# Optimization experiments

Measured on AMD Instinct MI355X. Metric: run time of the kernel, lower is better.

## Reference

```python
import jax, jax.numpy as jnp
import numpy as np

N = 50000   # nodes
E = 800000  # edges (avg degree 16)
H = 128     # hidden_dim / emb_dim
OUT = 128   # out_dim
NUM_BOND_TYPE = 6
NUM_BOND_DIR = 6


def setup_inputs() -> dict:
    key = jax.random.key(0)
    ks = jax.random.split(key, 12)
    s = 0.05
    return {
        "x": jax.random.normal(ks[0], (N, H), jnp.float32),
        "edge_index": jax.random.randint(ks[1], (2, E), 0, N),
        "edge_attr": jax.random.randint(ks[2], (E, 2), 0, 6),
        "prelu_a": jnp.float32(0.25),  # PReLU single shared slope (torch default)
        "W_enc": jax.random.normal(ks[3], (H, H), jnp.float32) * s,  # enc_to_dec, no bias
        "edge_emb1": jax.random.normal(ks[4], (NUM_BOND_TYPE, H), jnp.float32) * s,
        "edge_emb2": jax.random.normal(ks[5], (NUM_BOND_DIR, H), jnp.float32) * s,
        "W1": jax.random.normal(ks[6], (H, 2 * H), jnp.float32) * s,
        "b1": jnp.zeros((2 * H,), jnp.float32),
        "W2": jax.random.normal(ks[7], (2 * H, OUT), jnp.float32) * s,
        "b2": jnp.zeros((OUT,), jnp.float32),
    }


def reference(x, edge_index, edge_attr, prelu_a, W_enc, edge_emb1, edge_emb2, W1, b1, W2, b2):
    n = x.shape[0]
    # GNNDecoder: PReLU then enc_to_dec linear (no bias)
    x = jnp.where(x > 0, x, prelu_a * x)
    x = x @ W_enc

    # GINConv.forward: add self loops, self-loop edge_attr = [5, 0]
    loop = jnp.arange(n)
    src = jnp.concatenate([edge_index[0], loop])  # [E+N]
    dst = jnp.concatenate([edge_index[1], loop])  # [E+N]
    ea1 = jnp.concatenate([edge_attr[:, 0], jnp.full((n,), 5, edge_attr.dtype)])
    ea2 = jnp.concatenate([edge_attr[:, 1], jnp.zeros((n,), edge_attr.dtype)])

    # edge embedding lookup + gather-add message + scatter-add aggregate
    edge_emb = edge_emb1[ea1] + edge_emb2[ea2]          # [E+N, H]
    msg = x[src] + edge_emb                             # message(x_j, edge_attr)
    agg = jax.ops.segment_sum(msg, dst, num_segments=n)  # aggr='add'

    # update: MLP Linear(H,2H) -> SiLU -> Linear(2H,OUT)
    h = jax.nn.silu(agg @ W1 + b1)
    return h @ W2 + b2
```

## Files before the change

### kernel.cpp

```cpp
#include <hip/hip_runtime.h>

typedef unsigned short u16;
typedef unsigned int   u32;
typedef __attribute__((ext_vector_type(8))) short short8;
typedef __attribute__((ext_vector_type(4))) float f32x4;

#define MAXDEG 64
#define CAP    28
#define EB     4096

__device__ __forceinline__ float bl(u32 u){ union{u32 i; float f;} c; c.i = u << 16; return c.f; }
__device__ __forceinline__ float bh(u32 u){ union{u32 i; float f;} c; c.i = u & 0xffff0000u; return c.f; }
__device__ __forceinline__ u16 f2b(float f){
  union{float f; u32 i;} c; c.f = f;
  return (u16)((c.i + 0x8000u) >> 16);
}
__device__ __forceinline__ u32 pk2(float a, float b){
  union{float f; u32 i;} x, y; x.f = a; y.f = b;
  return ((x.i + 0x8000u) >> 16) | ((y.i + 0x8000u) & 0xffff0000u);
}

__device__ __forceinline__ void tr_tile(
    const float* __restrict__ in, int K, int Nn, u16* __restrict__ out,
    int k0, int n0, int t, u16* __restrict__ sT )
{
  #pragma unroll
  for (int rr = 0; rr < 4; rr++) {
    int row = (t >> 4) + rr * 16;
    int c4  = (t & 15) * 4;
    float4 v = *(const float4*)&in[(size_t)(k0 + row) * Nn + n0 + c4];
    sT[(c4 + 0) * 72 + row] = f2b(v.x);
    sT[(c4 + 1) * 72 + row] = f2b(v.y);
    sT[(c4 + 2) * 72 + row] = f2b(v.z);
    sT[(c4 + 3) * 72 + row] = f2b(v.w);
  }
  __syncthreads();
  #pragma unroll
  for (int ww = 0; ww < 2; ww++) {
    int nn = (t >> 3) + ww * 32;
    int c8 = (t & 7) * 8;
    uint4 val = *(const uint4*)&sT[nn * 72 + c8];
    *(uint4*)&out[(size_t)(n0 + nn) * K + k0 + c8] = val;
  }
}

__global__ __launch_bounds__(256) void k_prep(
    const float* __restrict__ Wenc, const float* __restrict__ W1,
    const float* __restrict__ W2, const float* __restrict__ e1,
    const float* __restrict__ e2, u16* __restrict__ WencT,
    u16* __restrict__ W1T, u16* __restrict__ W2T,
    u32* __restrict__ embP)
{
  __shared__ u16 sT[64 * 72];
  const int b = blockIdx.x, t = threadIdx.x;

  if (b < 4) {
    tr_tile(Wenc, 128, 128, WencT, (b & 1) * 64, (b >> 1) * 64, t, sT);
  } else if (b < 12) {
    int l = b - 4;
    tr_tile(W1, 128, 256, W1T, (l & 1) * 64, (l >> 1) * 64, t, sT);
  } else if (b < 20) {
    int l = b - 12;
    tr_tile(W2, 256, 128, W2T, (l & 3) * 64, (l >> 2) * 64, t, sT);
  } else {
    for (int i = t; i < 2304; i += 256) {
      int q = i / 576, rem = i - q * 576;
      int c = rem >> 4, s = rem & 15;
      int c1 = c / 6, c2 = c - c1 * 6;
      int col = q * 32 + s * 2;
      embP[i] = pk2(e1[c1 * 128 + col]     + e2[c2 * 128 + col],
                    e1[c1 * 128 + col + 1] + e2[c2 * 128 + col + 1]);
    }
  }
}

__global__ __launch_bounds__(256) void k_enc_count(
    const float* __restrict__ x, const float* __restrict__ pa,
    const u16* __restrict__ WT, u16* __restrict__ xencQ, int N,
    const int* __restrict__ ei, const int* __restrict__ ea,
    uint2* __restrict__ binned, int* __restrict__ bcnt,
    int E, int encBlocks, int nBuckets)
{
  if ((int)blockIdx.x >= encBlocks) {
    __shared__ int cntB[1024];
    const int t = threadIdx.x;
    const int blk = (int)blockIdx.x - encBlocks;
    for (int i = t; i < nBuckets; i += 256) cntB[i] = 0;
    __syncthreads();

    const int e0 = blk * EB;
    u32 recx[16]; int bkt[16], nl[16]; bool ok[16];
    #pragma unroll
    for (int j = 0; j < 16; j++) {
      int e = e0 + 256 * j + t;
      ok[j] = e < E;
      if (ok[j]) {
        int src = ei[e];
        int dst = ei[E + e];
        int2 a = *(const int2*)&ea[2 * e];
        recx[j] = (u32)src | ((u32)(a.x * 6 + a.y) << 26);
        bkt[j] = dst >> 6;
        nl[j]  = dst & 63;
      }
    }
    uint2* myRegion = binned + (size_t)blk * nBuckets * CAP;
    #pragma unroll
    for (int j = 0; j < 16; j++) {
      if (ok[j]) {
        int slot = atomicAdd(&cntB[bkt[j]], 1);
        if (slot < CAP)
          myRegion[bkt[j] * CAP + slot] = make_uint2(recx[j], (u32)nl[j]);
      }
    }
    __syncthreads();
    for (int i = t; i < nBuckets; i += 256)
      bcnt[blk * nBuckets + i] = min(cntB[i], CAP);
    return;
  }

  const int SK = 136, NT = 8;
  __shared__ u16 sB[128 * SK];

  const int t = threadIdx.x;
  #pragma unroll
  for (int j = 0; j < 8; j++) {
    int i = t + 256 * j;
    int n = i >> 4, k8 = i & 15;
    *(uint4*)&sB[n * SK + k8 * 8] = *(const uint4*)&WT[n * 128 + k8 * 8];
  }
  __syncthreads();

  const float slope = pa[0];
  const int lane = t & 63, wave = t >> 6, quad = lane >> 4, l16 = lane & 15;
  const int m0 = blockIdx.x * 128 + wave * 32;
  if (m0 >= N) return;

  f32x4 acc[2][NT];
  #pragma unroll
  for (int mr = 0; mr < 2; mr++)
    #pragma unroll
    for (int nt = 0; nt < NT; nt++) acc[mr][nt] = (f32x4){0.f, 0.f, 0.f, 0.f};

  #pragma unroll
  for (int ks = 0; ks < 4; ks++) {
    const int k0 = ks * 32 + quad * 8;
    union { u32 u[4]; short8 s; } a[2];
    #pragma unroll
    for (int mr = 0; mr < 2; mr++) {
      int row = m0 + mr * 16 + l16; row = min(row, N - 1);
      const float4* ap = (const float4*)&x[(size_t)row * 128 + k0];
      float4 f0 = ap[0], f1 = ap[1];
      float v0 = f0.x > 0.f ? f0.x : slope * f0.x;
      float v1 = f0.y > 0.f ? f0.y : slope * f0.y;
      float v2 = f0.z > 0.f ? f0.z : slope * f0.z;
      float v3 = f0.w > 0.f ? f0.w : slope * f0.w;
      float v4 = f1.x > 0.f ? f1.x : slope * f1.x;
      float v5 = f1.y > 0.f ? f1.y : slope * f1.y;
      float v6 = f1.z > 0.f ? f1.z : slope * f1.z;
      float v7 = f1.w > 0.f ? f1.w : slope * f1.w;
      a[mr].u[0] = pk2(v0, v1); a[mr].u[1] = pk2(v2, v3);
      a[mr].u[2] = pk2(v4, v5); a[mr].u[3] = pk2(v6, v7);
    }
    #pragma unroll
    for (int nt = 0; nt < NT; nt++) {
      short8 b = *(const short8*)&sB[(nt * 16 + l16) * SK + k0];
      acc[0][nt] = __builtin_amdgcn_mfma_f32_16x16x32_bf16(a[0].s, b, acc[0][nt], 0, 0, 0);
      acc[1][nt] = __builtin_amdgcn_mfma_f32_16x16x32_bf16(a[1].s, b, acc[1][nt], 0, 0, 0);
    }
  }

  #pragma unroll
  for (int mr = 0; mr < 2; mr++)
    #pragma unroll
    for (int nt = 0; nt < NT; nt++) {
      int col = nt * 16 + l16;
      int q = col >> 5, cq = col & 31;
      #pragma unroll
      for (int r = 0; r < 4; r++) {
        int row = m0 + mr * 16 + quad * 4 + r;
        if (row < N)
          xencQ[((size_t)q * N + row) * 32 + cq] = f2b(acc[mr][nt][r]);
      }
    }
}

__global__ __launch_bounds__(256) void k_place(
    const uint2* __restrict__ binned, const int* __restrict__ bcnt,
    u32* __restrict__ recs, int* __restrict__ cnt,
    int N, int nBlkA, int nBuckets)
{
  __shared__ int cntL[64];
  __shared__ int sBC[256];
  const int b = blockIdx.x, t = threadIdx.x;

  if (t < 64) cntL[t] = 0;
  const int nA = min(nBlkA, 256);
  if (t < nA) sBC[t] = bcnt[t * nBuckets + b];
  __syncthreads();

  const int total = nA * CAP;
  for (int i = t; i < total; i += 256) {
    int blk = i / CAP, j = i - blk * CAP;
    if (j < sBC[blk]) {
      uint2 r = binned[((size_t)blk * nBuckets + b) * CAP + j];
      int nl = (int)r.y;
      int slot = atomicAdd(&cntL[nl], 1);
      if (slot < MAXDEG)
        recs[(size_t)((b << 6) + nl) * MAXDEG + slot] = r.x;
    }
  }
  __syncthreads();

  if (t < 64) {
    int node = (b << 6) + t;
    if (node < N) cnt[node] = min(cntL[t], MAXDEG);
  }
}

struct B8 { uint2 x[8]; u32 r[8]; };

__device__ __forceinline__ void issue8(B8& b, u32 rv, int grp,
                                       const u32* __restrict__ xq, int sub) {
  #pragma unroll
  for (int k = 0; k < 8; k++) {
    u32 r = __shfl(rv, grp + k);
    b.r[k] = r;
    b.x[k] = *(const uint2*)&xq[(size_t)(r & 0x3ffffffu) * 16 + sub * 2];
  }
}

__device__ __forceinline__ void acc8(float* a, const B8& b,
                                     const u32* __restrict__ sEq,
                                     int sub, int dleft) {
  #pragma unroll
  for (int k = 0; k < 8; k++) {
    if (k < dleft) {
      uint2 e = *(const uint2*)&sEq[(b.r[k] >> 26) * 18 + sub * 2];
      uint2 x = b.x[k];
      a[0] += bl(x.x) + bl(e.x);  a[1] += bh(x.x) + bh(e.x);
      a[2] += bl(x.y) + bl(e.y);  a[3] += bh(x.y) + bh(e.y);
    }
  }
}

__global__ __launch_bounds__(256) void k_gather(
    const int* __restrict__ cnt, const u32* __restrict__ recs,
    const u32* __restrict__ embP, const u32* __restrict__ xencQ,
    u32* __restrict__ aggbQ, int N, int nodeBlocks)
{
  const int ES = 18;
  __shared__ u32 sE[36 * ES];

  const int t = threadIdx.x;
  const int q = (int)blockIdx.x / nodeBlocks;
  const int nbid = (int)blockIdx.x - q * nodeBlocks;

  for (int i = t; i < 576; i += 256) {
    int c = i >> 4, s = i & 15;
    sE[c * ES + s] = embP[q * 576 + i];
  }
  __syncthreads();

  const int lane = t & 63, wave = t >> 6;
  const int grp = lane & 56, sub = lane & 7;
  const int v = nbid * 32 + wave * 8 + (lane >> 3);
  const bool vok = v < N;
  const int vc = vok ? v : N - 1;
  const int d = vok ? min(cnt[vc], MAXDEG) : 0;
  const int beg = vc * MAXDEG;
  const int end = beg + d;

  u32 rv0 = 0, rv1 = 0, rv2 = 0, rv3 = 0;
  if (d > 0)  rv0 = recs[min(beg + sub, end - 1)];
  if (d > 8)  rv1 = recs[min(beg + 8 + sub, end - 1)];
  if (d > 16) rv2 = recs[min(beg + 16 + sub, end - 1)];
  if (d > 24) rv3 = recs[min(beg + 24 + sub, end - 1)];

  const u32* xq = xencQ + (size_t)q * N * 16;

  uint2 xs = *(const uint2*)&xq[(size_t)vc * 16 + sub * 2];
  uint2 es = *(const uint2*)&sE[30 * ES + sub * 2];
  float a[4];
  a[0] = bl(xs.x) + bl(es.x);  a[1] = bh(xs.x) + bh(es.x);
  a[2] = bl(xs.y) + bl(es.y);  a[3] = bh(xs.y) + bh(es.y);

  if (d > 0) {
    B8 bA, bB;
    issue8(bA, rv0, grp, xq, sub);
    if (d > 8) issue8(bB, rv1, grp, xq, sub);
    acc8(a, bA, sE, sub, d);
    if (d > 8) {
      if (d > 16) issue8(bA, rv2, grp, xq, sub);
      acc8(a, bB, sE, sub, d - 8);
      if (d > 16) {
        if (d > 24) issue8(bB, rv3, grp, xq, sub);
        acc8(a, bA, sE, sub, d - 16);
        if (d > 24) {
          acc8(a, bB, sE, sub, d - 24);
          for (int j0 = 32; j0 < d; j0 += 8) {
            u32 rvt = recs[min(beg + j0 + sub, end - 1)];
            issue8(bA, rvt, grp, xq, sub);
            acc8(a, bA, sE, sub, d - j0);
          }
        }
      }
    }
  }

  if (vok) {
    uint2 o;
    o.x = pk2(a[0], a[1]);
    o.y = pk2(a[2], a[3]);
    *(uint2*)&aggbQ[((size_t)q * N + vc) * 16 + sub * 2] = o;
  }
}

__global__ __launch_bounds__(256) void k_mlp(
    const u16* __restrict__ aggbQ, const u16* __restrict__ W1T,
    const float* __restrict__ b1, const u16* __restrict__ W2T,
    const float* __restrict__ b2, float* __restrict__ out, int N)
{
  const int SK = 136;
  __shared__ u16 sW[128 * SK];
  __shared__ u16 sH[128 * SK];
  __shared__ float sB1[256];
  __shared__ float sB2[128];

  const int t = threadIdx.x;
  const int lane = t & 63, wave = t >> 6, quad = lane >> 4, l16 = lane & 15;
  const int m0 = blockIdx.x * 128 + wave * 32;

  if (t < 128) sB2[t] = b2[t];
  sB1[t] = b1[t];

  union { uint4 q; short8 s; } a[2][4];
  #pragma unroll
  for (int mr = 0; mr < 2; mr++) {
    int row = min(m0 + mr * 16 + l16, N - 1);
    #pragma unroll
    for (int ks = 0; ks < 4; ks++)
      a[mr][ks].q = *(const uint4*)&aggbQ[((size_t)ks * N + row) * 32 + quad * 8];
  }

  f32x4 acc2[2][8];
  #pragma unroll
  for (int mr = 0; mr < 2; mr++)
    #pragma unroll
    for (int nt = 0; nt < 8; nt++) acc2[mr][nt] = (f32x4){0.f, 0.f, 0.f, 0.f};

  for (int half = 0; half < 2; half++) {
    #pragma unroll
    for (int j = 0; j < 8; j++) {
      int i = t + 256 * j;
      int n = i >> 4, k8 = i & 15;
      *(uint4*)&sW[n * SK + k8 * 8] =
          *(const uint4*)&W1T[(size_t)(half * 128 + n) * 128 + k8 * 8];
    }
    __syncthreads();

    f32x4 acc1[2][8];
    #pragma unroll
    for (int mr = 0; mr < 2; mr++)
      #pragma unroll
      for (int nt = 0; nt < 8; nt++) acc1[mr][nt] = (f32x4){0.f, 0.f, 0.f, 0.f};

    #pragma unroll
    for (int ks = 0; ks < 4; ks++) {
      const int k0 = ks * 32 + quad * 8;
      #pragma unroll
      for (int nt = 0; nt < 8; nt++) {
        short8 b = *(const short8*)&sW[(nt * 16 + l16) * SK + k0];
        acc1[0][nt] = __builtin_amdgcn_mfma_f32_16x16x32_bf16(a[0][ks].s, b, acc1[0][nt], 0, 0, 0);
        acc1[1][nt] = __builtin_amdgcn_mfma_f32_16x16x32_bf16(a[1][ks].s, b, acc1[1][nt], 0, 0, 0);
      }
    }

    #pragma unroll
    for (int mr = 0; mr < 2; mr++)
      #pragma unroll
      for (int nt = 0; nt < 8; nt++) {
        int col = nt * 16 + l16;
        float bias = sB1[half * 128 + col];
        #pragma unroll
        for (int r = 0; r < 4; r++) {
          float z = acc1[mr][nt][r] + bias;
          float s = z / (1.f + __expf(-z));
          sH[(wave * 32 + mr * 16 + quad * 4 + r) * SK + col] = f2b(s);
        }
      }
    __syncthreads();

    #pragma unroll
    for (int j = 0; j < 8; j++) {
      int i = t + 256 * j;
      int n = i >> 4, k8 = i & 15;
      *(uint4*)&sW[n * SK + k8 * 8] =
          *(const uint4*)&W2T[(size_t)n * 256 + half * 128 + k8 * 8];
    }
    __syncthreads();

    #pragma unroll
    for (int ks = 0; ks < 4; ks++) {
      const int k0 = ks * 32 + quad * 8;
      union { uint4 q; short8 s; } ah[2];
      #pragma unroll
      for (int mr = 0; mr < 2; mr++)
        ah[mr].q = *(const uint4*)&sH[(wave * 32 + mr * 16 + l16) * SK + k0];
      #pragma unroll
      for (int nt = 0; nt < 8; nt++) {
        short8 b = *(const short8*)&sW[(nt * 16 + l16) * SK + k0];
        acc2[0][nt] = __builtin_amdgcn_mfma_f32_16x16x32_bf16(ah[0].s, b, acc2[0][nt], 0, 0, 0);
        acc2[1][nt] = __builtin_amdgcn_mfma_f32_16x16x32_bf16(ah[1].s, b, acc2[1][nt], 0, 0, 0);
      }
    }
    __syncthreads();
  }

  #pragma unroll
  for (int mr = 0; mr < 2; mr++)
    #pragma unroll
    for (int nt = 0; nt < 8; nt++) {
      int col = nt * 16 + l16;
      float bias = sB2[col];
      #pragma unroll
      for (int r = 0; r < 4; r++) {
        int row = m0 + mr * 16 + quad * 4 + r;
        if (row < N) out[(size_t)row * 128 + col] = acc2[mr][nt][r] + bias;
      }
    }
}

extern "C" void kernel_launch(void* const* d_in, const int* in_sizes, int n_in,
                              void* d_out, int out_size, void* d_ws, size_t ws_size,
                              hipStream_t stream) {
  const float* x    = (const float*)d_in[0];
  const int*   ei   = (const int*)d_in[1];
  const int*   ea   = (const int*)d_in[2];
  const float* pa   = (const float*)d_in[3];
  const float* Wenc = (const float*)d_in[4];
  const float* e1   = (const float*)d_in[5];
  const float* e2   = (const float*)d_in[6];
  const float* W1   = (const float*)d_in[7];
  const float* b1   = (const float*)d_in[8];
  const float* W2   = (const float*)d_in[9];
  const float* b2   = (const float*)d_in[10];
  float* out = (float*)d_out;

  const int N = in_sizes[0] / 128;
  const int E = in_sizes[1] / 2;

  const int encBlocks  = (N + 127) / 128;
  const int nBlkA      = (E + EB - 1) / EB;
  const int nBuckets   = (N + 63) / 64;
  const int nodeBlocks = (N + 31) / 32;

  char* ws = (char*)d_ws;
  size_t off = 0;
  auto alloc = [&](size_t bytes) {
    void* p = ws + off;
    off = (off + bytes + 255) & ~(size_t)255;
    return p;
  };
  u16*   xencQ  = (u16*)  alloc((size_t)N * 128 * 2);
  u32*   aggbQ  = (u32*)  alloc((size_t)N * 64 * 4);
  int*   cnt    = (int*)  alloc((size_t)nBuckets * 64 * 4);
  u32*   recs   = (u32*)  alloc((size_t)nBuckets * 64 * MAXDEG * 4);
  uint2* binned = (uint2*)alloc((size_t)nBlkA * nBuckets * CAP * 8);
  int*   bcnt   = (int*)  alloc((size_t)nBlkA * nBuckets * 4);
  u16*   WencT  = (u16*)  alloc(128 * 128 * 2);
  u16*   W1T    = (u16*)  alloc(256 * 128 * 2);
  u16*   W2T    = (u16*)  alloc(128 * 256 * 2);
  u32*   embP   = (u32*)  alloc(2304 * 4);

  k_prep<<<21, 256, 0, stream>>>(Wenc, W1, W2, e1, e2,
                                 WencT, W1T, W2T, embP);
  k_enc_count<<<encBlocks + nBlkA, 256, 0, stream>>>(
      x, pa, WencT, xencQ, N, ei, ea, binned, bcnt, E, encBlocks, nBuckets);
  k_place<<<nBuckets, 256, 0, stream>>>(
      binned, bcnt, recs, cnt, N, nBlkA, nBuckets);
  k_gather<<<4 * nodeBlocks, 256, 0, stream>>>(
      cnt, recs, embP, (const u32*)xencQ, aggbQ, N, nodeBlocks);
  k_mlp<<<encBlocks, 256, 0, stream>>>(
      (const u16*)aggbQ, W1T, b1, W2T, b2, out, N);
}
```

Baseline: 194.6 us.

## Fuse bucket placement and gather into one kernel with LDS atomic accumulation

Removes the separate placement kernel and its global per-node record array. Each block takes one 64-node bucket and one feature quarter, loads that bucket's binned records into LDS, and gathers source features. It accumulates messages with shared-memory float atomics, then adds the self-loop and writes bf16 output. This saves one launch and a global write/read round trip, but every feature quarter re-reads the binned records (4x). It also adds LDS atomic contention, and buckets with more than 1344 records are silently truncated.

```diff
diff --git a/kernel.cpp b/kernel.cpp
--- a/kernel.cpp
+++ b/kernel.cpp
@@ -5,9 +5,9 @@
 typedef __attribute__((ext_vector_type(8))) short short8;
 typedef __attribute__((ext_vector_type(4))) float f32x4;
 
-#define MAXDEG 64
 #define CAP    28
 #define EB     4096
+#define RCAP   1344
 
 __device__ __forceinline__ float bl(u32 u){ union{u32 i; float f;} c; c.i = u << 16; return c.f; }
 __device__ __forceinline__ float bh(u32 u){ union{u32 i; float f;} c; c.i = u & 0xffff0000u; return c.f; }
@@ -184,134 +184,93 @@
     }
 }
 
-__global__ __launch_bounds__(256) void k_place(
+__global__ __launch_bounds__(256) void k_bgather(
     const uint2* __restrict__ binned, const int* __restrict__ bcnt,
-    u32* __restrict__ recs, int* __restrict__ cnt,
-    int N, int nBlkA, int nBuckets)
+    const u32* __restrict__ embP, const u32* __restrict__ xencQ,
+    u32* __restrict__ aggbQ, int N, int nBlkA, int nBuckets)
 {
-  __shared__ int cntL[64];
-  __shared__ int sBC[256];
-  const int b = blockIdx.x, t = threadIdx.x;
-
-  if (t < 64) cntL[t] = 0;
+  __shared__ float accQ[64 * 33];
+  __shared__ float embL[36 * 33];
+  __shared__ uint2 recL[RCAP];
+  __shared__ int   sBC[256];
+  __shared__ int   nRecS;
+
+  const int t = threadIdx.x;
+  const int q = (int)blockIdx.x / nBuckets;
+  const int b = (int)blockIdx.x - q * nBuckets;
+
+  for (int i = t; i < 64 * 33; i += 256) accQ[i] = 0.f;
+  for (int i = t; i < 576; i += 256) {
+    u32 p = embP[q * 576 + i];
+    int c = i >> 4, s = i & 15;
+    embL[c * 33 + s * 2]     = bl(p);
+    embL[c * 33 + s * 2 + 1] = bh(p);
+  }
   const int nA = min(nBlkA, 256);
   if (t < nA) sBC[t] = bcnt[t * nBuckets + b];
+  if (t == 0) nRecS = 0;
   __syncthreads();
 
   const int total = nA * CAP;
   for (int i = t; i < total; i += 256) {
     int blk = i / CAP, j = i - blk * CAP;
     if (j < sBC[blk]) {
-      uint2 r = binned[((size_t)blk * nBuckets + b) * CAP + j];
-      int nl = (int)r.y;
-      int slot = atomicAdd(&cntL[nl], 1);
-      if (slot < MAXDEG)
-        recs[(size_t)((b << 6) + nl) * MAXDEG + slot] = r.x;
-    }
-  }
-  __syncthreads();
-
-  if (t < 64) {
-    int node = (b << 6) + t;
-    if (node < N) cnt[node] = min(cntL[t], MAXDEG);
-  }
-}
-
-struct B8 { uint2 x[8]; u32 r[8]; };
-
-__device__ __forceinline__ void issue8(B8& b, u32 rv, int grp,
-                                       const u32* __restrict__ xq, int sub) {
-  #pragma unroll
-  for (int k = 0; k < 8; k++) {
-    u32 r = __shfl(rv, grp + k);
-    b.r[k] = r;
-    b.x[k] = *(const uint2*)&xq[(size_t)(r & 0x3ffffffu) * 16 + sub * 2];
-  }
-}
-
-__device__ __forceinline__ void acc8(float* a, const B8& b,
-                                     const u32* __restrict__ sEq,
-                                     int sub, int dleft) {
-  #pragma unroll
-  for (int k = 0; k < 8; k++) {
-    if (k < dleft) {
-      uint2 e = *(const uint2*)&sEq[(b.r[k] >> 26) * 18 + sub * 2];
-      uint2 x = b.x[k];
-      a[0] += bl(x.x) + bl(e.x);  a[1] += bh(x.x) + bh(e.x);
-      a[2] += bl(x.y) + bl(e.y);  a[3] += bh(x.y) + bh(e.y);
-    }
-  }
-}
-
-__global__ __launch_bounds__(256) void k_gather(
-    const int* __restrict__ cnt, const u32* __restrict__ recs,
-    const u32* __restrict__ embP, const u32* __restrict__ xencQ,
-    u32* __restrict__ aggbQ, int N, int nodeBlocks)
-{
-  const int ES = 18;
-  __shared__ u32 sE[36 * ES];
-
-  const int t = threadIdx.x;
-  const int q = (int)blockIdx.x / nodeBlocks;
-  const int nbid = (int)blockIdx.x - q * nodeBlocks;
-
-  for (int i = t; i < 576; i += 256) {
-    int c = i >> 4, s = i & 15;
-    sE[c * ES + s] = embP[q * 576 + i];
-  }
-  __syncthreads();
-
-  const int lane = t & 63, wave = t >> 6;
-  const int grp = lane & 56, sub = lane & 7;
-  const int v = nbid * 32 + wave * 8 + (lane >> 3);
-  const bool vok = v < N;
-  const int vc = vok ? v : N - 1;
-  const int d = vok ? min(cnt[vc], MAXDEG) : 0;
-  const int beg = vc * MAXDEG;
-  const int end = beg + d;
-
-  u32 rv0 = 0, rv1 = 0, rv2 = 0, rv3 = 0;
-  if (d > 0)  rv0 = recs[min(beg + sub, end - 1)];
-  if (d > 8)  rv1 = recs[min(beg + 8 + sub, end - 1)];
-  if (d > 16) rv2 = recs[min(beg + 16 + sub, end - 1)];
-  if (d > 24) rv3 = recs[min(beg + 24 + sub, end - 1)];
+      int s = atomicAdd(&nRecS, 1);
+      if (s < RCAP)
+        recL[s] = binned[((size_t)blk * nBuckets + b) * CAP + j];
+    }
+  }
+  __syncthreads();
+  const int nRec = min(nRecS, RCAP);
 
   const u32* xq = xencQ + (size_t)q * N * 16;
-
-  uint2 xs = *(const uint2*)&xq[(size_t)vc * 16 + sub * 2];
-  uint2 es = *(const uint2*)&sE[30 * ES + sub * 2];
-  float a[4];
-  a[0] = bl(xs.x) + bl(es.x);  a[1] = bh(xs.x) + bh(es.x);
-  a[2] = bl(xs.y) + bl(es.y);  a[3] = bh(xs.y) + bh(es.y);
-
-  if (d > 0) {
-    B8 bA, bB;
-    issue8(bA, rv0, grp, xq, sub);
-    if (d > 8) issue8(bB, rv1, grp, xq, sub);
-    acc8(a, bA, sE, sub, d);
-    if (d > 8) {
-      if (d > 16) issue8(bA, rv2, grp, xq, sub);
-      acc8(a, bB, sE, sub, d - 8);
-      if (d > 16) {
-        if (d > 24) issue8(bB, rv3, grp, xq, sub);
-        acc8(a, bA, sE, sub, d - 16);
-        if (d > 24) {
-          acc8(a, bB, sE, sub, d - 24);
-          for (int j0 = 32; j0 < d; j0 += 8) {
-            u32 rvt = recs[min(beg + j0 + sub, end - 1)];
-            issue8(bA, rvt, grp, xq, sub);
-            acc8(a, bA, sE, sub, d - j0);
-          }
-        }
-      }
-    }
-  }
-
-  if (vok) {
-    uint2 o;
-    o.x = pk2(a[0], a[1]);
-    o.y = pk2(a[2], a[3]);
-    *(uint2*)&aggbQ[((size_t)q * N + vc) * 16 + sub * 2] = o;
+  const int g = t >> 3, sub = t & 7;
+
+  uint2 recA = make_uint2(0u, 0u), xvA = make_uint2(0u, 0u);
+  if (g < nRec) {
+    recA = recL[g];
+    xvA = *(const uint2*)&xq[(size_t)(recA.x & 0x3ffffffu) * 16 + sub * 2];
+  }
+  for (int r = g; r < nRec; r += 32) {
+    int rn = r + 32;
+    uint2 recB = make_uint2(0u, 0u), xvB = make_uint2(0u, 0u);
+    if (rn < nRec) {
+      recB = recL[rn];
+      xvB = *(const uint2*)&xq[(size_t)(recB.x & 0x3ffffffu) * 16 + sub * 2];
+    }
+    const float* ef = &embL[(recA.x >> 26) * 33 + sub * 4];
+    float* ap = &accQ[(int)recA.y * 33 + sub * 4];
+    atomicAdd(&ap[0], bl(xvA.x) + ef[0]);
+    atomicAdd(&ap[1], bh(xvA.x) + ef[1]);
+    atomicAdd(&ap[2], bl(xvA.y) + ef[2]);
+    atomicAdd(&ap[3], bh(xvA.y) + ef[3]);
+    recA = recB; xvA = xvB;
+  }
+  __syncthreads();
+
+  #pragma unroll
+  for (int p = 0; p < 2; p++) {
+    int nl = p * 32 + g;
+    int node = b * 64 + nl;
+    if (node < N) {
+      uint2 xs = *(const uint2*)&xq[(size_t)node * 16 + sub * 2];
+      const float* ef = &embL[30 * 33 + sub * 4];
+      float* ap = &accQ[nl * 33 + sub * 4];
+      ap[0] += bl(xs.x) + ef[0];
+      ap[1] += bh(xs.x) + ef[1];
+      ap[2] += bl(xs.y) + ef[2];
+      ap[3] += bh(xs.y) + ef[3];
+    }
+  }
+  __syncthreads();
+
+  for (int i = t; i < 64 * 16; i += 256) {
+    int nl = i >> 4, s = i & 15;
+    int node = b * 64 + nl;
+    if (node < N) {
+      u32 o = pk2(accQ[nl * 33 + s * 2], accQ[nl * 33 + s * 2 + 1]);
+      aggbQ[((size_t)q * N + node) * 16 + s] = o;
+    }
   }
 }
 
@@ -449,10 +408,9 @@
   const int N = in_sizes[0] / 128;
   const int E = in_sizes[1] / 2;
 
-  const int encBlocks  = (N + 127) / 128;
-  const int nBlkA      = (E + EB - 1) / EB;
-  const int nBuckets   = (N + 63) / 64;
-  const int nodeBlocks = (N + 31) / 32;
+  const int encBlocks = (N + 127) / 128;
+  const int nBlkA     = (E + EB - 1) / EB;
+  const int nBuckets  = (N + 63) / 64;
 
   char* ws = (char*)d_ws;
   size_t off = 0;
@@ -463,8 +421,6 @@
   };
   u16*   xencQ  = (u16*)  alloc((size_t)N * 128 * 2);
   u32*   aggbQ  = (u32*)  alloc((size_t)N * 64 * 4);
-  int*   cnt    = (int*)  alloc((size_t)nBuckets * 64 * 4);
-  u32*   recs   = (u32*)  alloc((size_t)nBuckets * 64 * MAXDEG * 4);
   uint2* binned = (uint2*)alloc((size_t)nBlkA * nBuckets * CAP * 8);
   int*   bcnt   = (int*)  alloc((size_t)nBlkA * nBuckets * 4);
   u16*   WencT  = (u16*)  alloc(128 * 128 * 2);
@@ -476,10 +432,8 @@
                                  WencT, W1T, W2T, embP);
   k_enc_count<<<encBlocks + nBlkA, 256, 0, stream>>>(
       x, pa, WencT, xencQ, N, ei, ea, binned, bcnt, E, encBlocks, nBuckets);
-  k_place<<<nBuckets, 256, 0, stream>>>(
-      binned, bcnt, recs, cnt, N, nBlkA, nBuckets);
-  k_gather<<<4 * nodeBlocks, 256, 0, stream>>>(
-      cnt, recs, embP, (const u32*)xencQ, aggbQ, N, nodeBlocks);
+  k_bgather<<<4 * nBuckets, 256, 0, stream>>>(
+      binned, bcnt, embP, (const u32*)xencQ, aggbQ, N, nBlkA, nBuckets);
   k_mlp<<<encBlocks, 256, 0, stream>>>(
       (const u16*)aggbQ, W1T, b1, W2T, b2, out, N);
 }
```

New measurement: 719.7 us. +269.9%, slower.
